# Kernel optimization log

Measured on AMD Instinct MI355X. Metric: run time of the kernel, lower is better.

Reference implementation:

```python
import jax, jax.numpy as jnp
import numpy as np

B, F, H = 512, 64, 256
INPUT_LEN, TARGET_LEN = 128, 128


def _gru_step(h, xt, Wih, Whh, bih, bhh):
    # PyTorch GRU cell: gates ordered [r, z, n]
    gi = xt @ Wih.T + bih            # [B, 3H]
    gh = h @ Whh.T + bhh             # [B, 3H]
    ir, iz, inn = jnp.split(gi, 3, axis=-1)
    hr, hz, hn = jnp.split(gh, 3, axis=-1)
    r = jax.nn.sigmoid(ir + hr)
    z = jax.nn.sigmoid(iz + hz)
    n = jnp.tanh(inn + r * hn)
    return (1.0 - z) * n + z * h


def setup_inputs() -> dict:
    key = jax.random.key(0)
    ks = jax.random.split(key, 12)
    s_in = 1.0 / np.sqrt(H)
    x = jax.random.normal(ks[0], (B, INPUT_LEN + TARGET_LEN, F), dtype=jnp.float32)
    u = lambda k, shp: jax.random.uniform(k, shp, jnp.float32, -s_in, s_in)
    return {
        "x": x,
        "enc_Wih": u(ks[1], (3 * H, F)), "enc_Whh": u(ks[2], (3 * H, H)),
        "enc_bih": u(ks[3], (3 * H,)), "enc_bhh": u(ks[4], (3 * H,)),
        "dec_Wih": u(ks[5], (3 * H, F)), "dec_Whh": u(ks[6], (3 * H, H)),
        "dec_bih": u(ks[7], (3 * H,)), "dec_bhh": u(ks[8], (3 * H,)),
        "reg_W": u(ks[9], (F, H)), "reg_b": u(ks[10], (F,)),
        "input_len": INPUT_LEN, "target_len": TARGET_LEN,
    }


def reference(x, enc_Wih, enc_Whh, enc_bih, enc_bhh,
              dec_Wih, dec_Whh, dec_bih, dec_bhh,
              reg_W, reg_b, input_len, target_len):
    source_seq = x[:, :input_len, :]                       # [B, Tin, F]
    b = source_seq.shape[0]

    # Encoder GRU over source sequence, h0 = 0
    def enc_step(h, xt):
        h = _gru_step(h, xt, enc_Wih, enc_Whh, enc_bih, enc_bhh)
        return h, None
    h0 = jnp.zeros((b, enc_Whh.shape[1]), dtype=x.dtype)
    h_enc, _ = jax.lax.scan(enc_step, h0, source_seq.transpose(1, 0, 2))

    # Decoder: eval mode -> teacher forcing prob 0, always feed back own output
    dec_in0 = source_seq[:, -1, :]                         # [B, F]
    def dec_step(carry, _):
        h, inp = carry
        h = _gru_step(h, inp, dec_Wih, dec_Whh, dec_bih, dec_bhh)
        out = h @ reg_W.T + reg_b                          # [B, F]
        return (h, out), out
    (_, _), outs = jax.lax.scan(dec_step, (h_enc, dec_in0), None, length=target_len)
    return outs.transpose(1, 0, 2)                         # [B, Tout, F]
```

## Files before the change

kernel.cpp:

```cpp
#include <hip/hip_runtime.h>
#include <math.h>

#define Bsz 512
#define Fsz 64
#define Hsz 256
#define TSTEPS 128
#define G3 768

#define BG 16
#define HB 16
#define NBLK 256
#define NTHR 256
#define CNT_STRIDE 512
#define POLLER 192

#define AP 264
#define XAP 72

#define OFF_AH  0
#define OFF_AL  16896
#define OFF_XH  33792
#define OFF_XL  38400
#define OFF_RED 43008
#define OFF_B   75776
#define SMEM_BYTES (OFF_B + 512)

typedef float f32x4 __attribute__((ext_vector_type(4)));
typedef short s16x8 __attribute__((ext_vector_type(8)));
typedef unsigned short u16x4 __attribute__((ext_vector_type(4)));
typedef unsigned int  u32x4 __attribute__((ext_vector_type(4)));

#define MF(a,b,c) __builtin_amdgcn_mfma_f32_16x16x32_bf16(a,b,c,0,0,0)

static __device__ __forceinline__ unsigned short bf16_rne(float f){
    union { float f; unsigned u; } v; v.f = f;
    return (unsigned short)((v.u + 0x7FFFu + ((v.u >> 16) & 1u)) >> 16);
}
static __device__ __forceinline__ float bf16_to_f(unsigned short h){
    union { unsigned u; float f; } v; v.u = ((unsigned)h) << 16; return v.f;
}
static __device__ __forceinline__ void split8(const float* p, s16x8& hi, s16x8& lo){
    #pragma unroll
    for (int t = 0; t < 8; ++t){
        float f = p[t];
        unsigned short h = bf16_rne(f);
        hi[t] = (short)h;
        lo[t] = (short)bf16_rne(f - bf16_to_f(h));
    }
}
static __device__ __forceinline__ float sigmoidf_(float v){ return 1.0f/(1.0f + expf(-v)); }

__device__ __forceinline__ u32x4 load_sys_b128u(const unsigned* p){
    u32x4 r;
    asm volatile("global_load_dwordx4 %0, %1, off sc0 sc1" : "=v"(r) : "v"(p) : "memory");
    return r;
}
__device__ __forceinline__ void store_sys_b32u(unsigned* p, unsigned v){
    asm volatile("global_store_dword %0, %1, off sc0 sc1" :: "v"(p), "v"(v) : "memory");
}
__device__ __forceinline__ int load_sys_i32(const int* p){
    int r;
    asm volatile("global_load_dword %0, %1, off sc0 sc1\n\ts_waitcnt vmcnt(0)"
                 : "=v"(r) : "v"(p) : "memory");
    return r;
}
__device__ __forceinline__ void waitcnt0(){ asm volatile("s_waitcnt vmcnt(0)" ::: "memory"); }
__device__ __forceinline__ void regbar(u32x4& v){ asm volatile("" : "+v"(v)); }

extern "C" __global__ void gru_setup(const float* __restrict__ x,
                                     const float* __restrict__ dWih,
                                     const float* __restrict__ dbih,
                                     const float* __restrict__ regW,
                                     const float* __restrict__ regb,
                                     float* __restrict__ Mw,
                                     float* __restrict__ cfold,
                                     float* __restrict__ gi0)
{
    int idx = blockIdx.x*blockDim.x + threadIdx.x;
    if (idx < G3*Hsz) {
        int g = idx >> 8, j = idx & 255;
        float a = 0.f;
        #pragma unroll 8
        for (int f = 0; f < Fsz; ++f) a += dWih[g*Fsz + f]*regW[f*Hsz + j];
        Mw[idx] = a;
    } else if (idx < G3*Hsz + G3) {
        int g = idx - G3*Hsz;
        float a = dbih[g];
        #pragma unroll 8
        for (int f = 0; f < Fsz; ++f) a += dWih[g*Fsz + f]*regb[f];
        cfold[g] = a;
    } else {
        int e = idx - (G3*Hsz + G3);
        if (e < Bsz*G3) {
            int b = e / G3, g = e - b*G3;
            const float* xp = x + (size_t)b*(256*64) + 127*64;
            float a = dbih[g];
            #pragma unroll 8
            for (int f = 0; f < Fsz; ++f) a += xp[f]*dWih[g*Fsz + f];
            gi0[e] = a;
        }
    }
}

extern "C" __global__ void __launch_bounds__(NTHR, 1)
gru_persistent(const float* __restrict__ x,
               const float* __restrict__ eWih, const float* __restrict__ eWhh,
               const float* __restrict__ ebih, const float* __restrict__ ebhh,
               const float* __restrict__ dWhh, const float* __restrict__ dbhh,
               const float* __restrict__ Mw,   const float* __restrict__ cfold,
               const float* __restrict__ gi0,  const float* __restrict__ regW,
               const float* __restrict__ regb,
               unsigned* __restrict__ hbuf, int* __restrict__ cnt,
               float* __restrict__ out)
{
    extern __shared__ char lds[];
    unsigned short* s_ah = (unsigned short*)(lds + OFF_AH);
    unsigned short* s_al = (unsigned short*)(lds + OFF_AL);
    unsigned short* s_xh = (unsigned short*)(lds + OFF_XH);
    unsigned short* s_xl = (unsigned short*)(lds + OFF_XL);
    float* s_red  = (float*)(lds + OFF_RED);
    float* s_bias = (float*)(lds + OFF_B);
    float* s_dbh  = s_bias + 64;
    float* s_b3   = s_bias + 112;

    const int tid  = threadIdx.x;
    const int wv   = tid >> 6;
    const int lane = tid & 63;
    const int quad = lane >> 4;
    const int lcol = lane & 15;
    const int bg   = blockIdx.x >> 4;
    const int hb   = blockIdx.x & 15;
    const int hcol = hb*16 + lcol;
    int* mycnt = cnt + bg*CNT_STRIDE;
    const f32x4 z4 = {0.f, 0.f, 0.f, 0.f};

    s16x8 wfh[3][2], wfl[3][2];
    s16x8 ufh[3], ufl[3];
    #pragma unroll
    for (int g = 0; g < 3; ++g)
        #pragma unroll
        for (int q = 0; q < 2; ++q)
            split8(eWhh + (size_t)(g*256 + hcol)*256 + wv*64 + q*32 + quad*8,
                   wfh[g][q], wfl[g][q]);
    if (wv < 2){
        #pragma unroll
        for (int g = 0; g < 3; ++g)
            split8(eWih + (size_t)(g*256 + hcol)*64 + wv*32 + quad*8, ufh[g], ufl[g]);
    }
    if (tid < 16){
        int c = hb*16 + tid;
        s_bias[tid]    = ebih[c]       + ebhh[c];
        s_bias[16+tid] = ebih[256+c]   + ebhh[256+c];
        s_bias[32+tid] = ebih[512+c];
        s_bias[48+tid] = ebhh[512+c];
    }
    __syncthreads();

    int parity = 0;

    for (int s = 0; s < TSTEPS; ++s) {
        f32x4 aR[2], aZ[2], aNi[2], aNh[2];
        if (wv == 0){
            float bR = s_bias[lcol], bZ = s_bias[16+lcol];
            float bNi = s_bias[32+lcol], bNh = s_bias[48+lcol];
            #pragma unroll
            for (int m = 0; m < 2; ++m){
                aR[m] = (f32x4){bR,bR,bR,bR}; aZ[m] = (f32x4){bZ,bZ,bZ,bZ};
                aNi[m] = (f32x4){bNi,bNi,bNi,bNi}; aNh[m] = (f32x4){bNh,bNh,bNh,bNh};
            }
        } else {
            #pragma unroll
            for (int m = 0; m < 2; ++m){ aR[m]=z4; aZ[m]=z4; aNi[m]=z4; aNh[m]=z4; }
        }

        #pragma unroll
        for (int jj = 0; jj < 2; ++jj){
            int flat = (wv*2 + jj)*64 + lane;
            int row = flat >> 4, c4 = flat & 15;
            f32x4 xv = *(const f32x4*)(x + (size_t)(bg*32+row)*(256*64) + (size_t)s*64 + c4*4);
            u16x4 xh, xl;
            #pragma unroll
            for (int t = 0; t < 4; ++t){
                unsigned short h = bf16_rne(xv[t]);
                xh[t] = h; xl[t] = bf16_rne(xv[t] - bf16_to_f(h));
            }
            *(u16x4*)(s_xh + row*XAP + c4*4) = xh;
            *(u16x4*)(s_xl + row*XAP + c4*4) = xl;
        }
        __syncthreads();

        if (wv < 2){
            #pragma unroll
            for (int m = 0; m < 2; ++m){
                const int ko = wv*32 + quad*8;
                s16x8 xah = *(const s16x8*)(s_xh + (m*16+lcol)*XAP + ko);
                s16x8 xal = *(const s16x8*)(s_xl + (m*16+lcol)*XAP + ko);
                aR[m]=MF(xah,ufh[0],aR[m]); aR[m]=MF(xah,ufl[0],aR[m]); aR[m]=MF(xal,ufh[0],aR[m]);
                aZ[m]=MF(xah,ufh[1],aZ[m]); aZ[m]=MF(xah,ufl[1],aZ[m]); aZ[m]=MF(xal,ufh[1],aZ[m]);
                aNi[m]=MF(xah,ufh[2],aNi[m]); aNi[m]=MF(xah,ufl[2],aNi[m]); aNi[m]=MF(xal,ufh[2],aNi[m]);
            }
        }

        if (s > 0 && tid == POLLER){
            while (load_sys_i32(mycnt + s) < HB) __builtin_amdgcn_s_sleep(2);
        }
        __syncthreads();

        const unsigned* hin = hbuf + (size_t)parity*Bsz*Hsz;
        {
            u32x4 t[8];
            #pragma unroll
            for (int jj = 0; jj < 8; ++jj){
                int flat = (wv*8 + jj)*64 + lane;
                int row = flat >> 6, c4 = flat & 63;
                t[jj] = load_sys_b128u(hin + (size_t)(bg*32+row)*256 + c4*4);
            }
            waitcnt0();
            #pragma unroll
            for (int jj = 0; jj < 8; ++jj) regbar(t[jj]);
            #pragma unroll
            for (int jj = 0; jj < 8; ++jj){
                int flat = (wv*8 + jj)*64 + lane;
                int row = flat >> 6, c4 = flat & 63;
                u16x4 hh, ll;
                #pragma unroll
                for (int e = 0; e < 4; ++e){
                    unsigned u = t[jj][e];
                    hh[e] = (unsigned short)(u >> 16);
                    ll[e] = (unsigned short)(u & 0xFFFFu);
                }
                *(u16x4*)(s_ah + row*AP + c4*4) = hh;
                *(u16x4*)(s_al + row*AP + c4*4) = ll;
            }
        }
        __syncthreads();

        #pragma unroll
        for (int m = 0; m < 2; ++m){
            #pragma unroll
            for (int q = 0; q < 2; ++q){
                const int ko = wv*64 + q*32 + quad*8;
                s16x8 ah = *(const s16x8*)(s_ah + (m*16+lcol)*AP + ko);
                s16x8 al = *(const s16x8*)(s_al + (m*16+lcol)*AP + ko);
                aR[m]=MF(ah,wfh[0][q],aR[m]); aR[m]=MF(ah,wfl[0][q],aR[m]); aR[m]=MF(al,wfh[0][q],aR[m]);
                aZ[m]=MF(ah,wfh[1][q],aZ[m]); aZ[m]=MF(ah,wfl[1][q],aZ[m]); aZ[m]=MF(al,wfh[1][q],aZ[m]);
                aNh[m]=MF(ah,wfh[2][q],aNh[m]); aNh[m]=MF(ah,wfl[2][q],aNh[m]); aNh[m]=MF(al,wfh[2][q],aNh[m]);
            }
        }

        #pragma unroll
        for (int m = 0; m < 2; ++m){
            f32x4* rp = (f32x4*)s_red + (wv*8 + m*4)*64 + lane;
            rp[0] = aR[m]; rp[64] = aZ[m]; rp[128] = aNi[m]; rp[192] = aNh[m];
        }
        __syncthreads();

        unsigned* hout = hbuf + (size_t)(parity^1)*Bsz*Hsz;
        if (wv < 2){
            const int m = wv;
            f32x4 R = z4, Z = z4, Ni = z4, Nh = z4;
            #pragma unroll
            for (int w = 0; w < 4; ++w){
                const f32x4* rp = (const f32x4*)s_red + (w*8 + m*4)*64 + lane;
                R += rp[0]; Z += rp[64]; Ni += rp[128]; Nh += rp[192];
            }
            #pragma unroll
            for (int j = 0; j < 4; ++j){
                int rl = m*16 + quad*4 + j;
                float r = sigmoidf_(R[j]);
                float z = sigmoidf_(Z[j]);
                float n = tanhf(Ni[j] + r*Nh[j]);
                float hold = bf16_to_f(s_ah[rl*AP + hcol]) + bf16_to_f(s_al[rl*AP + hcol]);
                float hv = (1.0f - z)*n + z*hold;
                unsigned short p1 = bf16_rne(hv);
                unsigned short p0 = bf16_rne(hv - bf16_to_f(p1));
                store_sys_b32u(hout + (size_t)(bg*32+rl)*256 + hcol,
                               (((unsigned)p1) << 16) | (unsigned)p0);
            }
            waitcnt0();
        }
        __syncthreads();
        if (tid == POLLER)
            __hip_atomic_fetch_add(mycnt + s + 1, 1, __ATOMIC_RELAXED,
                                   __HIP_MEMORY_SCOPE_SYSTEM);
        parity ^= 1;
    }

    s16x8 mfh[3][2], mfl[3][2];
    #pragma unroll
    for (int g = 0; g < 3; ++g)
        #pragma unroll
        for (int q = 0; q < 2; ++q){
            split8(dWhh + (size_t)(g*256 + hcol)*256 + wv*64 + q*32 + quad*8,
                   wfh[g][q], wfl[g][q]);
            split8(Mw   + (size_t)(g*256 + hcol)*256 + wv*64 + q*32 + quad*8,
                   mfh[g][q], mfl[g][q]);
        }
    s16x8 rwh[8], rwl[8];
    if (wv >= 2){
        #pragma unroll
        for (int q8 = 0; q8 < 8; ++q8)
            split8(regW + (size_t)(hb*4 + (lcol & 3))*256 + q8*32 + quad*8,
                   rwh[q8], rwl[q8]);
    }
    if (tid < 16){
        int c = hb*16 + tid;
        s_bias[tid]    = cfold[c]     + dbhh[c];
        s_bias[16+tid] = cfold[256+c] + dbhh[256+c];
        s_bias[32+tid] = cfold[512+c];
        s_dbh[tid]     = dbhh[c];
        s_dbh[16+tid]  = dbhh[256+c];
        s_dbh[32+tid]  = dbhh[512+c];
    }
    if (tid < 4) s_b3[tid] = regb[hb*4 + tid];
    __syncthreads();

    for (int i = 0; i < TSTEPS; ++i) {
        const int sflag = TSTEPS + i;

        f32x4 aR[2], aZ[2], aNi[2], aNh[2];
        if (wv == 0){
            if (i == 0){
                #pragma unroll
                for (int m = 0; m < 2; ++m){
                    #pragma unroll
                    for (int j = 0; j < 4; ++j){
                        int grow_ = bg*32 + m*16 + quad*4 + j;
                        const float* gp = gi0 + (size_t)grow_*G3 + hcol;
                        aR[m][j]  = gp[0]   + s_dbh[lcol];
                        aZ[m][j]  = gp[256] + s_dbh[16+lcol];
                        aNi[m][j] = gp[512];
                        aNh[m][j] = s_dbh[32+lcol];
                    }
                }
            } else {
                float bR = s_bias[lcol], bZ = s_bias[16+lcol];
                float bNi = s_bias[32+lcol], bNh = s_dbh[32+lcol];
                #pragma unroll
                for (int m = 0; m < 2; ++m){
                    aR[m] = (f32x4){bR,bR,bR,bR}; aZ[m] = (f32x4){bZ,bZ,bZ,bZ};
                    aNi[m] = (f32x4){bNi,bNi,bNi,bNi}; aNh[m] = (f32x4){bNh,bNh,bNh,bNh};
                }
            }
        } else {
            #pragma unroll
            for (int m = 0; m < 2; ++m){ aR[m]=z4; aZ[m]=z4; aNi[m]=z4; aNh[m]=z4; }
        }

        if (tid == POLLER){
            while (load_sys_i32(mycnt + sflag) < HB) __builtin_amdgcn_s_sleep(2);
        }
        __syncthreads();

        const unsigned* hin = hbuf + (size_t)parity*Bsz*Hsz;
        {
            u32x4 t[8];
            #pragma unroll
            for (int jj = 0; jj < 8; ++jj){
                int flat = (wv*8 + jj)*64 + lane;
                int row = flat >> 6, c4 = flat & 63;
                t[jj] = load_sys_b128u(hin + (size_t)(bg*32+row)*256 + c4*4);
            }
            waitcnt0();
            #pragma unroll
            for (int jj = 0; jj < 8; ++jj) regbar(t[jj]);
            #pragma unroll
            for (int jj = 0; jj < 8; ++jj){
                int flat = (wv*8 + jj)*64 + lane;
                int row = flat >> 6, c4 = flat & 63;
                u16x4 hh, ll;
                #pragma unroll
                for (int e = 0; e < 4; ++e){
                    unsigned u = t[jj][e];
                    hh[e] = (unsigned short)(u >> 16);
                    ll[e] = (unsigned short)(u & 0xFFFFu);
                }
                *(u16x4*)(s_ah + row*AP + c4*4) = hh;
                *(u16x4*)(s_al + row*AP + c4*4) = ll;
            }
        }
        __syncthreads();

        #pragma unroll
        for (int m = 0; m < 2; ++m){
            #pragma unroll
            for (int q = 0; q < 2; ++q){
                const int ko = wv*64 + q*32 + quad*8;
                s16x8 ah = *(const s16x8*)(s_ah + (m*16+lcol)*AP + ko);
                s16x8 al = *(const s16x8*)(s_al + (m*16+lcol)*AP + ko);
                aR[m]=MF(ah,wfh[0][q],aR[m]); aR[m]=MF(ah,wfl[0][q],aR[m]); aR[m]=MF(al,wfh[0][q],aR[m]);
                aZ[m]=MF(ah,wfh[1][q],aZ[m]); aZ[m]=MF(ah,wfl[1][q],aZ[m]); aZ[m]=MF(al,wfh[1][q],aZ[m]);
                aNh[m]=MF(ah,wfh[2][q],aNh[m]); aNh[m]=MF(ah,wfl[2][q],aNh[m]); aNh[m]=MF(al,wfh[2][q],aNh[m]);
                if (i > 0){
                    aR[m]=MF(ah,mfh[0][q],aR[m]); aR[m]=MF(ah,mfl[0][q],aR[m]); aR[m]=MF(al,mfh[0][q],aR[m]);
                    aZ[m]=MF(ah,mfh[1][q],aZ[m]); aZ[m]=MF(ah,mfl[1][q],aZ[m]); aZ[m]=MF(al,mfh[1][q],aZ[m]);
                    aNi[m]=MF(ah,mfh[2][q],aNi[m]); aNi[m]=MF(ah,mfl[2][q],aNi[m]); aNi[m]=MF(al,mfh[2][q],aNi[m]);
                }
            }
        }

        #pragma unroll
        for (int m = 0; m < 2; ++m){
            f32x4* rp = (f32x4*)s_red + (wv*8 + m*4)*64 + lane;
            rp[0] = aR[m]; rp[64] = aZ[m]; rp[128] = aNi[m]; rp[192] = aNh[m];
        }
        __syncthreads();

        unsigned* hout = hbuf + (size_t)(parity^1)*Bsz*Hsz;
        if (wv < 2){
            const int m = wv;
            f32x4 R = z4, Z = z4, Ni = z4, Nh = z4;
            #pragma unroll
            for (int w = 0; w < 4; ++w){
                const f32x4* rp = (const f32x4*)s_red + (w*8 + m*4)*64 + lane;
                R += rp[0]; Z += rp[64]; Ni += rp[128]; Nh += rp[192];
            }
            #pragma unroll
            for (int j = 0; j < 4; ++j){
                int rl = m*16 + quad*4 + j;
                float r = sigmoidf_(R[j]);
                float z = sigmoidf_(Z[j]);
                float n = tanhf(Ni[j] + r*Nh[j]);
                float hold = bf16_to_f(s_ah[rl*AP + hcol]) + bf16_to_f(s_al[rl*AP + hcol]);
                float hv = (1.0f - z)*n + z*hold;
                unsigned short p1 = bf16_rne(hv);
                unsigned short p0 = bf16_rne(hv - bf16_to_f(p1));
                store_sys_b32u(hout + (size_t)(bg*32+rl)*256 + hcol,
                               (((unsigned)p1) << 16) | (unsigned)p0);
            }
            waitcnt0();
        } else if (i >= 1){
            const int m = wv - 2;
            float b3 = s_b3[lcol & 3];
            f32x4 oa = (f32x4){b3, b3, b3, b3};
            #pragma unroll
            for (int q8 = 0; q8 < 8; ++q8){
                const int ko = q8*32 + quad*8;
                s16x8 ah = *(const s16x8*)(s_ah + (m*16+lcol)*AP + ko);
                s16x8 al = *(const s16x8*)(s_al + (m*16+lcol)*AP + ko);
                oa = MF(ah, rwh[q8], oa); oa = MF(ah, rwl[q8], oa); oa = MF(al, rwh[q8], oa);
            }
            if (lcol < 4){
                #pragma unroll
                for (int j = 0; j < 4; ++j)
                    out[(size_t)(bg*32 + m*16 + quad*4 + j)*(TSTEPS*Fsz)
                        + (size_t)(i-1)*Fsz + hb*4 + lcol] = oa[j];
            }
        }
        __syncthreads();
        if (tid == POLLER)
            __hip_atomic_fetch_add(mycnt + sflag + 1, 1, __ATOMIC_RELAXED,
                                   __HIP_MEMORY_SCOPE_SYSTEM);
        parity ^= 1;
    }

    {
        if (tid == POLLER){
            while (load_sys_i32(mycnt + 2*TSTEPS) < HB) __builtin_amdgcn_s_sleep(2);
        }
        __syncthreads();
        const unsigned* hin = hbuf + (size_t)parity*Bsz*Hsz;
        {
            u32x4 t[8];
            #pragma unroll
            for (int jj = 0; jj < 8; ++jj){
                int flat = (wv*8 + jj)*64 + lane;
                int row = flat >> 6, c4 = flat & 63;
                t[jj] = load_sys_b128u(hin + (size_t)(bg*32+row)*256 + c4*4);
            }
            waitcnt0();
            #pragma unroll
            for (int jj = 0; jj < 8; ++jj) regbar(t[jj]);
            #pragma unroll
            for (int jj = 0; jj < 8; ++jj){
                int flat = (wv*8 + jj)*64 + lane;
                int row = flat >> 6, c4 = flat & 63;
                u16x4 hh, ll;
                #pragma unroll
                for (int e = 0; e < 4; ++e){
                    unsigned u = t[jj][e];
                    hh[e] = (unsigned short)(u >> 16);
                    ll[e] = (unsigned short)(u & 0xFFFFu);
                }
                *(u16x4*)(s_ah + row*AP + c4*4) = hh;
                *(u16x4*)(s_al + row*AP + c4*4) = ll;
            }
        }
        __syncthreads();
        if (wv >= 2){
            const int m = wv - 2;
            float b3 = s_b3[lcol & 3];
            f32x4 oa = (f32x4){b3, b3, b3, b3};
            #pragma unroll
            for (int q8 = 0; q8 < 8; ++q8){
                const int ko = q8*32 + quad*8;
                s16x8 ah = *(const s16x8*)(s_ah + (m*16+lcol)*AP + ko);
                s16x8 al = *(const s16x8*)(s_al + (m*16+lcol)*AP + ko);
                oa = MF(ah, rwh[q8], oa); oa = MF(ah, rwl[q8], oa); oa = MF(al, rwh[q8], oa);
            }
            if (lcol < 4){
                #pragma unroll
                for (int j = 0; j < 4; ++j)
                    out[(size_t)(bg*32 + m*16 + quad*4 + j)*(TSTEPS*Fsz)
                        + (size_t)(TSTEPS-1)*Fsz + hb*4 + lcol] = oa[j];
            }
        }
    }
}

extern "C" void kernel_launch(void* const* d_in, const int* in_sizes, int n_in,
                              void* d_out, int out_size, void* d_ws, size_t ws_size,
                              hipStream_t stream)
{
    (void)in_sizes; (void)n_in; (void)out_size; (void)ws_size;
    const float* x    = (const float*)d_in[0];
    const float* eWih = (const float*)d_in[1];
    const float* eWhh = (const float*)d_in[2];
    const float* ebih = (const float*)d_in[3];
    const float* ebhh = (const float*)d_in[4];
    const float* dWih = (const float*)d_in[5];
    const float* dWhh = (const float*)d_in[6];
    const float* dbih = (const float*)d_in[7];
    const float* dbhh = (const float*)d_in[8];
    const float* regW = (const float*)d_in[9];
    const float* regb = (const float*)d_in[10];
    float* out = (float*)d_out;

    unsigned* hbuf = (unsigned*)d_ws;
    float* Mw    = (float*)d_ws + 2*Bsz*Hsz;
    float* gi0   = Mw + G3*Hsz;
    float* cfold = gi0 + Bsz*G3;
    int*   cnt   = (int*)(cfold + 1024);

    hipMemsetAsync(hbuf, 0, (size_t)Bsz*Hsz*sizeof(unsigned), stream);
    hipMemsetAsync(cnt, 0, (size_t)BG*CNT_STRIDE*sizeof(int), stream);

    hipLaunchKernelGGL(gru_setup, dim3(2307), dim3(256), 0, stream,
                       x, dWih, dbih, regW, regb, Mw, cfold, gi0);

    hipFuncSetAttribute((const void*)gru_persistent,
                        hipFuncAttributeMaxDynamicSharedMemorySize, SMEM_BYTES);

    void* args[] = { (void*)&x, (void*)&eWih, (void*)&eWhh, (void*)&ebih, (void*)&ebhh,
                     (void*)&dWhh, (void*)&dbhh, (void*)&Mw, (void*)&cfold, (void*)&gi0,
                     (void*)&regW, (void*)&regb, (void*)&hbuf, (void*)&cnt, (void*)&out };
    hipError_t rc = hipLaunchCooperativeKernel((const void*)gru_persistent,
                                               dim3(NBLK), dim3(NTHR), args,
                                               SMEM_BYTES, stream);
    if (rc != hipSuccess) {
        hipLaunchKernelGGL(gru_persistent, dim3(NBLK), dim3(NTHR), SMEM_BYTES, stream,
                           x, eWih, eWhh, ebih, ebhh, dWhh, dbhh, Mw, cfold, gi0,
                           regW, regb, hbuf, cnt, out);
    }
}
```

Before: 1.185 ms.

## Replace counter barrier with per-wave tags and direct register loads of h

Reworks the persistent GRU step loop. The per-group atomic counter polled by one thread, together with several block-wide __syncthreads per step, is replaced by per-block/half tag words that every wave polls itself. Each wave now loads its own hidden-state rows straight from global memory into registers instead of staging them through LDS. The K dimension is split across wave pairs with a small LDS partial-sum handoff guarded by a workgroup-scope flag, which cuts intra-block barriers and LDS traffic on the serial critical path. The risks are extra redundant global polling and loads, and more register pressure from holding twice as many weight fragments per wave.

```diff
diff --git a/kernel.cpp b/kernel.cpp
--- a/kernel.cpp
+++ b/kernel.cpp
@@ -11,24 +11,10 @@
 #define HB 16
 #define NBLK 256
 #define NTHR 256
-#define CNT_STRIDE 512
-#define POLLER 192
-
-#define AP 264
-#define XAP 72
-
-#define OFF_AH  0
-#define OFF_AL  16896
-#define OFF_XH  33792
-#define OFF_XL  38400
-#define OFF_RED 43008
-#define OFF_B   75776
-#define SMEM_BYTES (OFF_B + 512)
 
 typedef float f32x4 __attribute__((ext_vector_type(4)));
 typedef short s16x8 __attribute__((ext_vector_type(8)));
-typedef unsigned short u16x4 __attribute__((ext_vector_type(4)));
-typedef unsigned int  u32x4 __attribute__((ext_vector_type(4)));
+typedef unsigned int u32x4 __attribute__((ext_vector_type(4)));
 
 #define MF(a,b,c) __builtin_amdgcn_mfma_f32_16x16x32_bf16(a,b,c,0,0,0)
 
@@ -40,19 +26,46 @@
     union { unsigned u; float f; } v; v.u = ((unsigned)h) << 16; return v.f;
 }
 static __device__ __forceinline__ void split8(const float* p, s16x8& hi, s16x8& lo){
+    union { s16x8 v; unsigned short e[8]; } H, L;
     #pragma unroll
     for (int t = 0; t < 8; ++t){
         float f = p[t];
         unsigned short h = bf16_rne(f);
-        hi[t] = (short)h;
-        lo[t] = (short)bf16_rne(f - bf16_to_f(h));
-    }
+        H.e[t] = h; L.e[t] = bf16_rne(f - bf16_to_f(h));
+    }
+    hi = H.v; lo = L.v;
+}
+static __device__ __forceinline__ void split8f(f32x4 a, f32x4 b, s16x8& hi, s16x8& lo){
+    union { s16x8 v; unsigned short e[8]; } H, L;
+    float fv[8] = {a[0],a[1],a[2],a[3],b[0],b[1],b[2],b[3]};
+    #pragma unroll
+    for (int t = 0; t < 8; ++t){
+        unsigned short h = bf16_rne(fv[t]);
+        H.e[t] = h; L.e[t] = bf16_rne(fv[t] - bf16_to_f(h));
+    }
+    hi = H.v; lo = L.v;
+}
+static __device__ __forceinline__ void unpack8(u32x4 a, u32x4 b, s16x8& hi, s16x8& lo){
+    union { s16x8 v; unsigned u[4]; } H, L;
+    unsigned w[8] = {a[0],a[1],a[2],a[3],b[0],b[1],b[2],b[3]};
+    #pragma unroll
+    for (int d = 0; d < 4; ++d){
+        unsigned w0 = w[2*d], w1 = w[2*d+1];
+        H.u[d] = (w0 >> 16) | (w1 & 0xFFFF0000u);
+        L.u[d] = (w0 & 0xFFFFu) | (w1 << 16);
+    }
+    hi = H.v; lo = L.v;
 }
 static __device__ __forceinline__ float sigmoidf_(float v){ return 1.0f/(1.0f + expf(-v)); }
 
 __device__ __forceinline__ u32x4 load_sys_b128u(const unsigned* p){
     u32x4 r;
     asm volatile("global_load_dwordx4 %0, %1, off sc0 sc1" : "=v"(r) : "v"(p) : "memory");
+    return r;
+}
+__device__ __forceinline__ unsigned load_sys_b32u_async(const unsigned* p){
+    unsigned r;
+    asm volatile("global_load_dword %0, %1, off sc0 sc1" : "=v"(r) : "v"(p) : "memory");
     return r;
 }
 __device__ __forceinline__ void store_sys_b32u(unsigned* p, unsigned v){
@@ -65,7 +78,13 @@
     return r;
 }
 __device__ __forceinline__ void waitcnt0(){ asm volatile("s_waitcnt vmcnt(0)" ::: "memory"); }
-__device__ __forceinline__ void regbar(u32x4& v){ asm volatile("" : "+v"(v)); }
+__device__ __forceinline__ void regbar4(u32x4& v){ asm volatile("" : "+v"(v)); }
+__device__ __forceinline__ void regbar1(unsigned& v){ asm volatile("" : "+v"(v)); }
+
+__device__ __forceinline__ void poll_ge(const int* tp, int target){
+    int v;
+    do { v = load_sys_i32(tp); } while (!__all(v >= target));
+}
 
 extern "C" __global__ void gru_setup(const float* __restrict__ x,
                                      const float* __restrict__ dWih,
@@ -110,400 +129,315 @@
                const float* __restrict__ Mw,   const float* __restrict__ cfold,
                const float* __restrict__ gi0,  const float* __restrict__ regW,
                const float* __restrict__ regb,
-               unsigned* __restrict__ hbuf, int* __restrict__ cnt,
+               unsigned* __restrict__ hbuf, int* __restrict__ tags,
                float* __restrict__ out)
 {
-    extern __shared__ char lds[];
-    unsigned short* s_ah = (unsigned short*)(lds + OFF_AH);
-    unsigned short* s_al = (unsigned short*)(lds + OFF_AL);
-    unsigned short* s_xh = (unsigned short*)(lds + OFF_XH);
-    unsigned short* s_xl = (unsigned short*)(lds + OFF_XL);
-    float* s_red  = (float*)(lds + OFF_RED);
-    float* s_bias = (float*)(lds + OFF_B);
-    float* s_dbh  = s_bias + 64;
-    float* s_b3   = s_bias + 112;
+    __shared__ float s_part[4][4][256];
+    __shared__ float s_bias[128];
+    __shared__ unsigned short s_rw[2][8][64][8];
+    __shared__ int s_flag[2];
 
     const int tid  = threadIdx.x;
     const int wv   = tid >> 6;
+    const int m    = wv & 1;
+    const int kh   = wv >> 1;
     const int lane = tid & 63;
     const int quad = lane >> 4;
     const int lcol = lane & 15;
     const int bg   = blockIdx.x >> 4;
     const int hb   = blockIdx.x & 15;
     const int hcol = hb*16 + lcol;
-    int* mycnt = cnt + bg*CNT_STRIDE;
-    const f32x4 z4 = {0.f, 0.f, 0.f, 0.f};
-
-    s16x8 wfh[3][2], wfl[3][2];
+    const int* mytags = tags + bg*32;
+    const f32x4 z4 = {0.f,0.f,0.f,0.f};
+
+    s16x8 wfh[3][4], wfl[3][4];
     s16x8 ufh[3], ufl[3];
     #pragma unroll
-    for (int g = 0; g < 3; ++g)
-        #pragma unroll
-        for (int q = 0; q < 2; ++q)
-            split8(eWhh + (size_t)(g*256 + hcol)*256 + wv*64 + q*32 + quad*8,
-                   wfh[g][q], wfl[g][q]);
-    if (wv < 2){
-        #pragma unroll
-        for (int g = 0; g < 3; ++g)
-            split8(eWih + (size_t)(g*256 + hcol)*64 + wv*32 + quad*8, ufh[g], ufl[g]);
-    }
+    for (int g3 = 0; g3 < 3; ++g3){
+        #pragma unroll
+        for (int q = 0; q < 4; ++q)
+            split8(eWhh + (size_t)(g3*256 + hcol)*256 + kh*128 + q*32 + quad*8,
+                   wfh[g3][q], wfl[g3][q]);
+        split8(eWih + (size_t)(g3*256 + hcol)*64 + kh*32 + quad*8, ufh[g3], ufl[g3]);
+    }
+    if (tid == 0){ s_flag[0] = 0; s_flag[1] = 0; }
     if (tid < 16){
         int c = hb*16 + tid;
-        s_bias[tid]    = ebih[c]       + ebhh[c];
-        s_bias[16+tid] = ebih[256+c]   + ebhh[256+c];
+        s_bias[tid]    = ebih[c]     + ebhh[c];
+        s_bias[16+tid] = ebih[256+c] + ebhh[256+c];
         s_bias[32+tid] = ebih[512+c];
         s_bias[48+tid] = ebhh[512+c];
     }
     __syncthreads();
 
-    int parity = 0;
-
-    for (int s = 0; s < TSTEPS; ++s) {
-        f32x4 aR[2], aZ[2], aNi[2], aNh[2];
-        if (wv == 0){
-            float bR = s_bias[lcol], bZ = s_bias[16+lcol];
-            float bNi = s_bias[32+lcol], bNh = s_bias[48+lcol];
-            #pragma unroll
-            for (int m = 0; m < 2; ++m){
-                aR[m] = (f32x4){bR,bR,bR,bR}; aZ[m] = (f32x4){bZ,bZ,bZ,bZ};
-                aNi[m] = (f32x4){bNi,bNi,bNi,bNi}; aNh[m] = (f32x4){bNh,bNh,bNh,bNh};
-            }
+    for (int g = 0; g < TSTEPS; ++g){
+        const unsigned* hin  = hbuf + (size_t)(g & 1)*Bsz*Hsz;
+        unsigned* hout = hbuf + (size_t)((g + 1) & 1)*Bsz*Hsz;
+
+        f32x4 accR = z4, accZ = z4, accNi = z4, accNh = z4;
+
+        {
+            const float* xp = x + (size_t)(bg*32 + m*16 + lcol)*(256*64)
+                              + (size_t)g*64 + kh*32 + quad*8;
+            f32x4 xa = *(const f32x4*)xp;
+            f32x4 xb = *(const f32x4*)(xp + 4);
+            s16x8 xh, xl; split8f(xa, xb, xh, xl);
+            accR  = MF(xh, ufh[0], accR);  accR  = MF(xh, ufl[0], accR);  accR  = MF(xl, ufh[0], accR);
+            accZ  = MF(xh, ufh[1], accZ);  accZ  = MF(xh, ufl[1], accZ);  accZ  = MF(xl, ufh[1], accZ);
+            accNi = MF(xh, ufh[2], accNi); accNi = MF(xh, ufl[2], accNi); accNi = MF(xl, ufh[2], accNi);
+        }
+
+        if (g > 0) poll_ge(mytags + (lane & 31), g);
+
+        const unsigned* hrow = hin + (size_t)(bg*32 + m*16 + lcol)*256;
+        u32x4 A[8];
+        #pragma unroll
+        for (int q = 0; q < 4; ++q){
+            int ko = kh*128 + q*32 + quad*8;
+            A[2*q]   = load_sys_b128u(hrow + ko);
+            A[2*q+1] = load_sys_b128u(hrow + ko + 4);
+        }
+        unsigned HO[4];
+        if (kh == 0){
+            #pragma unroll
+            for (int j = 0; j < 4; ++j)
+                HO[j] = load_sys_b32u_async(hin + (size_t)(bg*32 + m*16 + quad*4 + j)*256 + hcol);
+        }
+        waitcnt0();
+        #pragma unroll
+        for (int q = 0; q < 8; ++q) regbar4(A[q]);
+        if (kh == 0){ regbar1(HO[0]); regbar1(HO[1]); regbar1(HO[2]); regbar1(HO[3]); }
+
+        s16x8 ah[4], al[4];
+        #pragma unroll
+        for (int q = 0; q < 4; ++q) unpack8(A[2*q], A[2*q+1], ah[q], al[q]);
+
+        #pragma unroll
+        for (int q = 0; q < 4; ++q){
+            s16x8 H = ah[q], L = al[q];
+            accR  = MF(H, wfh[0][q], accR);  accR  = MF(H, wfl[0][q], accR);  accR  = MF(L, wfh[0][q], accR);
+            accZ  = MF(H, wfh[1][q], accZ);  accZ  = MF(H, wfl[1][q], accZ);  accZ  = MF(L, wfh[1][q], accZ);
+            accNh = MF(H, wfh[2][q], accNh); accNh = MF(H, wfl[2][q], accNh); accNh = MF(L, wfh[2][q], accNh);
+        }
+
+        const int par = g & 1;
+        if (kh == 1){
+            float* pb = &s_part[m*2 + par][0][0] + lane*4;
+            *(f32x4*)(pb)       = accR;
+            *(f32x4*)(pb + 256) = accZ;
+            *(f32x4*)(pb + 512) = accNi;
+            *(f32x4*)(pb + 768) = accNh;
+            if (lane == 0)
+                __hip_atomic_store(&s_flag[m], g + 1, __ATOMIC_RELEASE, __HIP_MEMORY_SCOPE_WORKGROUP);
         } else {
-            #pragma unroll
-            for (int m = 0; m < 2; ++m){ aR[m]=z4; aZ[m]=z4; aNi[m]=z4; aNh[m]=z4; }
-        }
-
-        #pragma unroll
-        for (int jj = 0; jj < 2; ++jj){
-            int flat = (wv*2 + jj)*64 + lane;
-            int row = flat >> 4, c4 = flat & 15;
-            f32x4 xv = *(const f32x4*)(x + (size_t)(bg*32+row)*(256*64) + (size_t)s*64 + c4*4);
-            u16x4 xh, xl;
-            #pragma unroll
-            for (int t = 0; t < 4; ++t){
-                unsigned short h = bf16_rne(xv[t]);
-                xh[t] = h; xl[t] = bf16_rne(xv[t] - bf16_to_f(h));
-            }
-            *(u16x4*)(s_xh + row*XAP + c4*4) = xh;
-            *(u16x4*)(s_xl + row*XAP + c4*4) = xl;
-        }
-        __syncthreads();
-
-        if (wv < 2){
-            #pragma unroll
-            for (int m = 0; m < 2; ++m){
-                const int ko = wv*32 + quad*8;
-                s16x8 xah = *(const s16x8*)(s_xh + (m*16+lcol)*XAP + ko);
-                s16x8 xal = *(const s16x8*)(s_xl + (m*16+lcol)*XAP + ko);
-                aR[m]=MF(xah,ufh[0],aR[m]); aR[m]=MF(xah,ufl[0],aR[m]); aR[m]=MF(xal,ufh[0],aR[m]);
-                aZ[m]=MF(xah,ufh[1],aZ[m]); aZ[m]=MF(xah,ufl[1],aZ[m]); aZ[m]=MF(xal,ufh[1],aZ[m]);
-                aNi[m]=MF(xah,ufh[2],aNi[m]); aNi[m]=MF(xah,ufl[2],aNi[m]); aNi[m]=MF(xal,ufh[2],aNi[m]);
-            }
-        }
-
-        if (s > 0 && tid == POLLER){
-            while (load_sys_i32(mycnt + s) < HB) __builtin_amdgcn_s_sleep(2);
-        }
-        __syncthreads();
-
-        const unsigned* hin = hbuf + (size_t)parity*Bsz*Hsz;
-        {
-            u32x4 t[8];
-            #pragma unroll
-            for (int jj = 0; jj < 8; ++jj){
-                int flat = (wv*8 + jj)*64 + lane;
-                int row = flat >> 6, c4 = flat & 63;
-                t[jj] = load_sys_b128u(hin + (size_t)(bg*32+row)*256 + c4*4);
-            }
-            waitcnt0();
-            #pragma unroll
-            for (int jj = 0; jj < 8; ++jj) regbar(t[jj]);
-            #pragma unroll
-            for (int jj = 0; jj < 8; ++jj){
-                int flat = (wv*8 + jj)*64 + lane;
-                int row = flat >> 6, c4 = flat & 63;
-                u16x4 hh, ll;
-                #pragma unroll
-                for (int e = 0; e < 4; ++e){
-                    unsigned u = t[jj][e];
-                    hh[e] = (unsigned short)(u >> 16);
-                    ll[e] = (unsigned short)(u & 0xFFFFu);
-                }
-                *(u16x4*)(s_ah + row*AP + c4*4) = hh;
-                *(u16x4*)(s_al + row*AP + c4*4) = ll;
-            }
-        }
-        __syncthreads();
-
-        #pragma unroll
-        for (int m = 0; m < 2; ++m){
-            #pragma unroll
-            for (int q = 0; q < 2; ++q){
-                const int ko = wv*64 + q*32 + quad*8;
-                s16x8 ah = *(const s16x8*)(s_ah + (m*16+lcol)*AP + ko);
-                s16x8 al = *(const s16x8*)(s_al + (m*16+lcol)*AP + ko);
-                aR[m]=MF(ah,wfh[0][q],aR[m]); aR[m]=MF(ah,wfl[0][q],aR[m]); aR[m]=MF(al,wfh[0][q],aR[m]);
-                aZ[m]=MF(ah,wfh[1][q],aZ[m]); aZ[m]=MF(ah,wfl[1][q],aZ[m]); aZ[m]=MF(al,wfh[1][q],aZ[m]);
-                aNh[m]=MF(ah,wfh[2][q],aNh[m]); aNh[m]=MF(ah,wfl[2][q],aNh[m]); aNh[m]=MF(al,wfh[2][q],aNh[m]);
-            }
-        }
-
-        #pragma unroll
-        for (int m = 0; m < 2; ++m){
-            f32x4* rp = (f32x4*)s_red + (wv*8 + m*4)*64 + lane;
-            rp[0] = aR[m]; rp[64] = aZ[m]; rp[128] = aNi[m]; rp[192] = aNh[m];
-        }
-        __syncthreads();
-
-        unsigned* hout = hbuf + (size_t)(parity^1)*Bsz*Hsz;
-        if (wv < 2){
-            const int m = wv;
-            f32x4 R = z4, Z = z4, Ni = z4, Nh = z4;
-            #pragma unroll
-            for (int w = 0; w < 4; ++w){
-                const f32x4* rp = (const f32x4*)s_red + (w*8 + m*4)*64 + lane;
-                R += rp[0]; Z += rp[64]; Ni += rp[128]; Nh += rp[192];
-            }
+            while (__hip_atomic_load(&s_flag[m], __ATOMIC_ACQUIRE, __HIP_MEMORY_SCOPE_WORKGROUP) < g + 1) {}
+            const float* pb = &s_part[m*2 + par][0][0] + lane*4;
+            accR  += *(const f32x4*)(pb);
+            accZ  += *(const f32x4*)(pb + 256);
+            accNi += *(const f32x4*)(pb + 512);
+            accNh += *(const f32x4*)(pb + 768);
             #pragma unroll
             for (int j = 0; j < 4; ++j){
-                int rl = m*16 + quad*4 + j;
-                float r = sigmoidf_(R[j]);
-                float z = sigmoidf_(Z[j]);
-                float n = tanhf(Ni[j] + r*Nh[j]);
-                float hold = bf16_to_f(s_ah[rl*AP + hcol]) + bf16_to_f(s_al[rl*AP + hcol]);
-                float hv = (1.0f - z)*n + z*hold;
+                float R = sigmoidf_(accR[j] + s_bias[lcol]);
+                float Z = sigmoidf_(accZ[j] + s_bias[16 + lcol]);
+                float N = tanhf(accNi[j] + s_bias[32 + lcol] + R*(accNh[j] + s_bias[48 + lcol]));
+                float hold = bf16_to_f((unsigned short)(HO[j] >> 16))
+                           + bf16_to_f((unsigned short)(HO[j] & 0xFFFFu));
+                float hv = (1.0f - Z)*N + Z*hold;
                 unsigned short p1 = bf16_rne(hv);
                 unsigned short p0 = bf16_rne(hv - bf16_to_f(p1));
-                store_sys_b32u(hout + (size_t)(bg*32+rl)*256 + hcol,
+                store_sys_b32u(hout + (size_t)(bg*32 + m*16 + quad*4 + j)*256 + hcol,
                                (((unsigned)p1) << 16) | (unsigned)p0);
             }
             waitcnt0();
-        }
-        __syncthreads();
-        if (tid == POLLER)
-            __hip_atomic_fetch_add(mycnt + s + 1, 1, __ATOMIC_RELAXED,
-                                   __HIP_MEMORY_SCOPE_SYSTEM);
-        parity ^= 1;
-    }
-
-    s16x8 mfh[3][2], mfl[3][2];
+            if (lane == 0)
+                store_sys_b32u((unsigned*)(tags + bg*32 + hb*2 + m), (unsigned)(g + 1));
+        }
+    }
+
+    __syncthreads();
+    s16x8 mfh[3][4], mfl[3][4];
     #pragma unroll
-    for (int g = 0; g < 3; ++g)
-        #pragma unroll
-        for (int q = 0; q < 2; ++q){
-            split8(dWhh + (size_t)(g*256 + hcol)*256 + wv*64 + q*32 + quad*8,
-                   wfh[g][q], wfl[g][q]);
-            split8(Mw   + (size_t)(g*256 + hcol)*256 + wv*64 + q*32 + quad*8,
-                   mfh[g][q], mfl[g][q]);
-        }
-    s16x8 rwh[8], rwl[8];
-    if (wv >= 2){
-        #pragma unroll
-        for (int q8 = 0; q8 < 8; ++q8)
-            split8(regW + (size_t)(hb*4 + (lcol & 3))*256 + q8*32 + quad*8,
-                   rwh[q8], rwl[q8]);
+    for (int g3 = 0; g3 < 3; ++g3)
+        #pragma unroll
+        for (int q = 0; q < 4; ++q){
+            split8(dWhh + (size_t)(g3*256 + hcol)*256 + kh*128 + q*32 + quad*8,
+                   wfh[g3][q], wfl[g3][q]);
+            split8(Mw   + (size_t)(g3*256 + hcol)*256 + kh*128 + q*32 + quad*8,
+                   mfh[g3][q], mfl[g3][q]);
+        }
+    if (wv == 2){
+        #pragma unroll
+        for (int q8 = 0; q8 < 8; ++q8){
+            s16x8 rh, rl;
+            split8(regW + (size_t)(hb*4 + (lcol & 3))*256 + q8*32 + quad*8, rh, rl);
+            *(s16x8*)&s_rw[0][q8][lane][0] = rh;
+            *(s16x8*)&s_rw[1][q8][lane][0] = rl;
+        }
     }
     if (tid < 16){
         int c = hb*16 + tid;
-        s_bias[tid]    = cfold[c]     + dbhh[c];
-        s_bias[16+tid] = cfold[256+c] + dbhh[256+c];
-        s_bias[32+tid] = cfold[512+c];
-        s_dbh[tid]     = dbhh[c];
-        s_dbh[16+tid]  = dbhh[256+c];
-        s_dbh[32+tid]  = dbhh[512+c];
-    }
-    if (tid < 4) s_b3[tid] = regb[hb*4 + tid];
+        s_bias[tid]      = cfold[c]       + dbhh[c];
+        s_bias[16+tid]   = cfold[256+c]   + dbhh[256+c];
+        s_bias[32+tid]   = cfold[512+c];
+        s_bias[48+tid]   = dbhh[512+c];
+        s_bias[64+tid]   = dbhh[c];
+        s_bias[80+tid]   = dbhh[256+c];
+    }
+    if (tid < 4) s_bias[96 + tid] = regb[hb*4 + tid];
     __syncthreads();
 
-    for (int i = 0; i < TSTEPS; ++i) {
-        const int sflag = TSTEPS + i;
-
-        f32x4 aR[2], aZ[2], aNi[2], aNh[2];
-        if (wv == 0){
-            if (i == 0){
+    for (int i = 0; i < TSTEPS; ++i){
+        const int g = TSTEPS + i;
+        const unsigned* hin  = hbuf + (size_t)(g & 1)*Bsz*Hsz;
+        unsigned* hout = hbuf + (size_t)((g + 1) & 1)*Bsz*Hsz;
+
+        f32x4 accR = z4, accZ = z4, accNi = z4, accNh = z4;
+
+        poll_ge(mytags + (lane & 31), g);
+
+        const unsigned* hrow = hin + (size_t)(bg*32 + m*16 + lcol)*256;
+        u32x4 A[8], B2[8];
+        #pragma unroll
+        for (int q = 0; q < 4; ++q){
+            int ko = kh*128 + q*32 + quad*8;
+            A[2*q]   = load_sys_b128u(hrow + ko);
+            A[2*q+1] = load_sys_b128u(hrow + ko + 4);
+        }
+        unsigned HO[4];
+        if (kh == 0){
+            #pragma unroll
+            for (int j = 0; j < 4; ++j)
+                HO[j] = load_sys_b32u_async(hin + (size_t)(bg*32 + m*16 + quad*4 + j)*256 + hcol);
+        } else if (i >= 1){
+            #pragma unroll
+            for (int q = 0; q < 4; ++q){
+                int ko = q*32 + quad*8;
+                B2[2*q]   = load_sys_b128u(hrow + ko);
+                B2[2*q+1] = load_sys_b128u(hrow + ko + 4);
+            }
+        }
+        waitcnt0();
+        #pragma unroll
+        for (int q = 0; q < 8; ++q) regbar4(A[q]);
+        if (kh == 0){ regbar1(HO[0]); regbar1(HO[1]); regbar1(HO[2]); regbar1(HO[3]); }
+        else if (i >= 1){
+            #pragma unroll
+            for (int q = 0; q < 8; ++q) regbar4(B2[q]);
+        }
+
+        s16x8 ah[4], al[4];
+        #pragma unroll
+        for (int q = 0; q < 4; ++q) unpack8(A[2*q], A[2*q+1], ah[q], al[q]);
+
+        #pragma unroll
+        for (int q = 0; q < 4; ++q){
+            s16x8 H = ah[q], L = al[q];
+            accR  = MF(H, wfh[0][q], accR);  accR  = MF(H, wfl[0][q], accR);  accR  = MF(L, wfh[0][q], accR);
+            accZ  = MF(H, wfh[1][q], accZ);  accZ  = MF(H, wfl[1][q], accZ);  accZ  = MF(L, wfh[1][q], accZ);
+            accNh = MF(H, wfh[2][q], accNh); accNh = MF(H, wfl[2][q], accNh); accNh = MF(L, wfh[2][q], accNh);
+        }
+        if (i > 0){
+            #pragma unroll
+            for (int q = 0; q < 4; ++q){
+                s16x8 H = ah[q], L = al[q];
+                accR  = MF(H, mfh[0][q], accR);  accR  = MF(H, mfl[0][q], accR);  accR  = MF(L, mfh[0][q], accR);
+                accZ  = MF(H, mfh[1][q], accZ);  accZ  = MF(H, mfl[1][q], accZ);  accZ  = MF(L, mfh[1][q], accZ);
+                accNi = MF(H, mfh[2][q], accNi); accNi = MF(H, mfl[2][q], accNi); accNi = MF(L, mfh[2][q], accNi);
+            }
+        }
+
+        const int par = g & 1;
+        if (kh == 1){
+            float* pb = &s_part[m*2 + par][0][0] + lane*4;
+            *(f32x4*)(pb)       = accR;
+            *(f32x4*)(pb + 256) = accZ;
+            *(f32x4*)(pb + 512) = accNi;
+            *(f32x4*)(pb + 768) = accNh;
+            if (lane == 0)
+                __hip_atomic_store(&s_flag[m], g + 1, __ATOMIC_RELEASE, __HIP_MEMORY_SCOPE_WORKGROUP);
+            if (i >= 1){
+                s16x8 bh[4], bl[4];
                 #pragma unroll
-                for (int m = 0; m < 2; ++m){
+                for (int q = 0; q < 4; ++q) unpack8(B2[2*q], B2[2*q+1], bh[q], bl[q]);
+                float b3 = s_bias[96 + (lcol & 3)];
+                f32x4 oa = (f32x4){b3, b3, b3, b3};
+                #pragma unroll
+                for (int q8 = 0; q8 < 8; ++q8){
+                    s16x8 H = (q8 < 4) ? bh[q8] : ah[q8-4];
+                    s16x8 L = (q8 < 4) ? bl[q8] : al[q8-4];
+                    s16x8 rh = *(const s16x8*)&s_rw[0][q8][lane][0];
+                    s16x8 rl = *(const s16x8*)&s_rw[1][q8][lane][0];
+                    oa = MF(H, rh, oa); oa = MF(H, rl, oa); oa = MF(L, rh, oa);
+                }
+                if (lcol < 4){
                     #pragma unroll
-                    for (int j = 0; j < 4; ++j){
-                        int grow_ = bg*32 + m*16 + quad*4 + j;
-                        const float* gp = gi0 + (size_t)grow_*G3 + hcol;
-                        aR[m][j]  = gp[0]   + s_dbh[lcol];
-                        aZ[m][j]  = gp[256] + s_dbh[16+lcol];
-                        aNi[m][j] = gp[512];
-                        aNh[m][j] = s_dbh[32+lcol];
-                    }
-                }
-            } else {
-                float bR = s_bias[lcol], bZ = s_bias[16+lcol];
-                float bNi = s_bias[32+lcol], bNh = s_dbh[32+lcol];
-                #pragma unroll
-                for (int m = 0; m < 2; ++m){
-                    aR[m] = (f32x4){bR,bR,bR,bR}; aZ[m] = (f32x4){bZ,bZ,bZ,bZ};
-                    aNi[m] = (f32x4){bNi,bNi,bNi,bNi}; aNh[m] = (f32x4){bNh,bNh,bNh,bNh};
+                    for (int j = 0; j < 4; ++j)
+                        out[(size_t)(bg*32 + m*16 + quad*4 + j)*(TSTEPS*Fsz)
+                            + (size_t)(i-1)*Fsz + hb*4 + lcol] = oa[j];
                 }
             }
         } else {
-            #pragma unroll
-            for (int m = 0; m < 2; ++m){ aR[m]=z4; aZ[m]=z4; aNi[m]=z4; aNh[m]=z4; }
-        }
-
-        if (tid == POLLER){
-            while (load_sys_i32(mycnt + sflag) < HB) __builtin_amdgcn_s_sleep(2);
-        }
-        __syncthreads();
-
-        const unsigned* hin = hbuf + (size_t)parity*Bsz*Hsz;
-        {
-            u32x4 t[8];
-            #pragma unroll
-            for (int jj = 0; jj < 8; ++jj){
-                int flat = (wv*8 + jj)*64 + lane;
-                int row = flat >> 6, c4 = flat & 63;
-                t[jj] = load_sys_b128u(hin + (size_t)(bg*32+row)*256 + c4*4);
-            }
-            waitcnt0();
-            #pragma unroll
-            for (int jj = 0; jj < 8; ++jj) regbar(t[jj]);
-            #pragma unroll
-            for (int jj = 0; jj < 8; ++jj){
-                int flat = (wv*8 + jj)*64 + lane;
-                int row = flat >> 6, c4 = flat & 63;
-                u16x4 hh, ll;
-                #pragma unroll
-                for (int e = 0; e < 4; ++e){
-                    unsigned u = t[jj][e];
-                    hh[e] = (unsigned short)(u >> 16);
-                    ll[e] = (unsigned short)(u & 0xFFFFu);
+            while (__hip_atomic_load(&s_flag[m], __ATOMIC_ACQUIRE, __HIP_MEMORY_SCOPE_WORKGROUP) < g + 1) {}
+            const float* pb = &s_part[m*2 + par][0][0] + lane*4;
+            accR  += *(const f32x4*)(pb);
+            accZ  += *(const f32x4*)(pb + 256);
+            accNi += *(const f32x4*)(pb + 512);
+            accNh += *(const f32x4*)(pb + 768);
+            #pragma unroll
+            for (int j = 0; j < 4; ++j){
+                float R, Z, N;
+                if (i == 0){
+                    const float* gp = gi0 + (size_t)(bg*32 + m*16 + quad*4 + j)*G3 + hcol;
+                    R = sigmoidf_(accR[j] + gp[0]   + s_bias[64 + lcol]);
+                    Z = sigmoidf_(accZ[j] + gp[256] + s_bias[80 + lcol]);
+                    N = tanhf(accNi[j] + gp[512] + R*(accNh[j] + s_bias[48 + lcol]));
+                } else {
+                    R = sigmoidf_(accR[j] + s_bias[lcol]);
+                    Z = sigmoidf_(accZ[j] + s_bias[16 + lcol]);
+                    N = tanhf(accNi[j] + s_bias[32 + lcol] + R*(accNh[j] + s_bias[48 + lcol]));
                 }
-                *(u16x4*)(s_ah + row*AP + c4*4) = hh;
-                *(u16x4*)(s_al + row*AP + c4*4) = ll;
-            }
-        }
-        __syncthreads();
-
-        #pragma unroll
-        for (int m = 0; m < 2; ++m){
-            #pragma unroll
-            for (int q = 0; q < 2; ++q){
-                const int ko = wv*64 + q*32 + quad*8;
-                s16x8 ah = *(const s16x8*)(s_ah + (m*16+lcol)*AP + ko);
-                s16x8 al = *(const s16x8*)(s_al + (m*16+lcol)*AP + ko);
-                aR[m]=MF(ah,wfh[0][q],aR[m]); aR[m]=MF(ah,wfl[0][q],aR[m]); aR[m]=MF(al,wfh[0][q],aR[m]);
-                aZ[m]=MF(ah,wfh[1][q],aZ[m]); aZ[m]=MF(ah,wfl[1][q],aZ[m]); aZ[m]=MF(al,wfh[1][q],aZ[m]);
-                aNh[m]=MF(ah,wfh[2][q],aNh[m]); aNh[m]=MF(ah,wfl[2][q],aNh[m]); aNh[m]=MF(al,wfh[2][q],aNh[m]);
-                if (i > 0){
-                    aR[m]=MF(ah,mfh[0][q],aR[m]); aR[m]=MF(ah,mfl[0][q],aR[m]); aR[m]=MF(al,mfh[0][q],aR[m]);
-                    aZ[m]=MF(ah,mfh[1][q],aZ[m]); aZ[m]=MF(ah,mfl[1][q],aZ[m]); aZ[m]=MF(al,mfh[1][q],aZ[m]);
-                    aNi[m]=MF(ah,mfh[2][q],aNi[m]); aNi[m]=MF(ah,mfl[2][q],aNi[m]); aNi[m]=MF(al,mfh[2][q],aNi[m]);
-                }
-            }
-        }
-
-        #pragma unroll
-        for (int m = 0; m < 2; ++m){
-            f32x4* rp = (f32x4*)s_red + (wv*8 + m*4)*64 + lane;
-            rp[0] = aR[m]; rp[64] = aZ[m]; rp[128] = aNi[m]; rp[192] = aNh[m];
-        }
-        __syncthreads();
-
-        unsigned* hout = hbuf + (size_t)(parity^1)*Bsz*Hsz;
-        if (wv < 2){
-            const int m = wv;
-            f32x4 R = z4, Z = z4, Ni = z4, Nh = z4;
-            #pragma unroll
-            for (int w = 0; w < 4; ++w){
-                const f32x4* rp = (const f32x4*)s_red + (w*8 + m*4)*64 + lane;
-                R += rp[0]; Z += rp[64]; Ni += rp[128]; Nh += rp[192];
-            }
-            #pragma unroll
-            for (int j = 0; j < 4; ++j){
-                int rl = m*16 + quad*4 + j;
-                float r = sigmoidf_(R[j]);
-                float z = sigmoidf_(Z[j]);
-                float n = tanhf(Ni[j] + r*Nh[j]);
-                float hold = bf16_to_f(s_ah[rl*AP + hcol]) + bf16_to_f(s_al[rl*AP + hcol]);
-                float hv = (1.0f - z)*n + z*hold;
+                float hold = bf16_to_f((unsigned short)(HO[j] >> 16))
+                           + bf16_to_f((unsigned short)(HO[j] & 0xFFFFu));
+                float hv = (1.0f - Z)*N + Z*hold;
                 unsigned short p1 = bf16_rne(hv);
                 unsigned short p0 = bf16_rne(hv - bf16_to_f(p1));
-                store_sys_b32u(hout + (size_t)(bg*32+rl)*256 + hcol,
+                store_sys_b32u(hout + (size_t)(bg*32 + m*16 + quad*4 + j)*256 + hcol,
                                (((unsigned)p1) << 16) | (unsigned)p0);
             }
             waitcnt0();
-        } else if (i >= 1){
-            const int m = wv - 2;
-            float b3 = s_b3[lcol & 3];
-            f32x4 oa = (f32x4){b3, b3, b3, b3};
-            #pragma unroll
-            for (int q8 = 0; q8 < 8; ++q8){
-                const int ko = q8*32 + quad*8;
-                s16x8 ah = *(const s16x8*)(s_ah + (m*16+lcol)*AP + ko);
-                s16x8 al = *(const s16x8*)(s_al + (m*16+lcol)*AP + ko);
-                oa = MF(ah, rwh[q8], oa); oa = MF(ah, rwl[q8], oa); oa = MF(al, rwh[q8], oa);
-            }
-            if (lcol < 4){
-                #pragma unroll
-                for (int j = 0; j < 4; ++j)
-                    out[(size_t)(bg*32 + m*16 + quad*4 + j)*(TSTEPS*Fsz)
-                        + (size_t)(i-1)*Fsz + hb*4 + lcol] = oa[j];
-            }
-        }
-        __syncthreads();
-        if (tid == POLLER)
-            __hip_atomic_fetch_add(mycnt + sflag + 1, 1, __ATOMIC_RELAXED,
-                                   __HIP_MEMORY_SCOPE_SYSTEM);
-        parity ^= 1;
-    }
-
-    {
-        if (tid == POLLER){
-            while (load_sys_i32(mycnt + 2*TSTEPS) < HB) __builtin_amdgcn_s_sleep(2);
-        }
-        __syncthreads();
-        const unsigned* hin = hbuf + (size_t)parity*Bsz*Hsz;
-        {
-            u32x4 t[8];
-            #pragma unroll
-            for (int jj = 0; jj < 8; ++jj){
-                int flat = (wv*8 + jj)*64 + lane;
-                int row = flat >> 6, c4 = flat & 63;
-                t[jj] = load_sys_b128u(hin + (size_t)(bg*32+row)*256 + c4*4);
-            }
-            waitcnt0();
-            #pragma unroll
-            for (int jj = 0; jj < 8; ++jj) regbar(t[jj]);
-            #pragma unroll
-            for (int jj = 0; jj < 8; ++jj){
-                int flat = (wv*8 + jj)*64 + lane;
-                int row = flat >> 6, c4 = flat & 63;
-                u16x4 hh, ll;
-                #pragma unroll
-                for (int e = 0; e < 4; ++e){
-                    unsigned u = t[jj][e];
-                    hh[e] = (unsigned short)(u >> 16);
-                    ll[e] = (unsigned short)(u & 0xFFFFu);
-                }
-                *(u16x4*)(s_ah + row*AP + c4*4) = hh;
-                *(u16x4*)(s_al + row*AP + c4*4) = ll;
-            }
-        }
-        __syncthreads();
-        if (wv >= 2){
-            const int m = wv - 2;
-            float b3 = s_b3[lcol & 3];
-            f32x4 oa = (f32x4){b3, b3, b3, b3};
-            #pragma unroll
-            for (int q8 = 0; q8 < 8; ++q8){
-                const int ko = q8*32 + quad*8;
-                s16x8 ah = *(const s16x8*)(s_ah + (m*16+lcol)*AP + ko);
-                s16x8 al = *(const s16x8*)(s_al + (m*16+lcol)*AP + ko);
-                oa = MF(ah, rwh[q8], oa); oa = MF(ah, rwl[q8], oa); oa = MF(al, rwh[q8], oa);
-            }
-            if (lcol < 4){
-                #pragma unroll
-                for (int j = 0; j < 4; ++j)
-                    out[(size_t)(bg*32 + m*16 + quad*4 + j)*(TSTEPS*Fsz)
-                        + (size_t)(TSTEPS-1)*Fsz + hb*4 + lcol] = oa[j];
-            }
+            if (lane == 0)
+                store_sys_b32u((unsigned*)(tags + bg*32 + hb*2 + m), (unsigned)(g + 1));
+        }
+    }
+
+    if (kh == 1){
+        poll_ge(mytags + (lane & 31), 2*TSTEPS);
+        const unsigned* hrow = hbuf + (size_t)(bg*32 + m*16 + lcol)*256;
+        u32x4 C[16];
+        #pragma unroll
+        for (int q8 = 0; q8 < 8; ++q8){
+            int ko = q8*32 + quad*8;
+            C[2*q8]   = load_sys_b128u(hrow + ko);
+            C[2*q8+1] = load_sys_b128u(hrow + ko + 4);
+        }
+        waitcnt0();
+        #pragma unroll
+        for (int q = 0; q < 16; ++q) regbar4(C[q]);
+        float b3 = s_bias[96 + (lcol & 3)];
+        f32x4 oa = (f32x4){b3, b3, b3, b3};
+        #pragma unroll
+        for (int q8 = 0; q8 < 8; ++q8){
+            s16x8 H, L; unpack8(C[2*q8], C[2*q8+1], H, L);
+            s16x8 rh = *(const s16x8*)&s_rw[0][q8][lane][0];
+            s16x8 rl = *(const s16x8*)&s_rw[1][q8][lane][0];
+            oa = MF(H, rh, oa); oa = MF(H, rl, oa); oa = MF(L, rh, oa);
+        }
+        if (lcol < 4){
+            #pragma unroll
+            for (int j = 0; j < 4; ++j)
+                out[(size_t)(bg*32 + m*16 + quad*4 + j)*(TSTEPS*Fsz)
+                    + (size_t)(TSTEPS-1)*Fsz + hb*4 + lcol] = oa[j];
         }
     }
 }
@@ -530,26 +464,22 @@
     float* Mw    = (float*)d_ws + 2*Bsz*Hsz;
     float* gi0   = Mw + G3*Hsz;
     float* cfold = gi0 + Bsz*G3;
-    int*   cnt   = (int*)(cfold + 1024);
+    int*   tags  = (int*)(cfold + 1024);
 
     hipMemsetAsync(hbuf, 0, (size_t)Bsz*Hsz*sizeof(unsigned), stream);
-    hipMemsetAsync(cnt, 0, (size_t)BG*CNT_STRIDE*sizeof(int), stream);
+    hipMemsetAsync(tags, 0, (size_t)BG*32*sizeof(int), stream);
 
     hipLaunchKernelGGL(gru_setup, dim3(2307), dim3(256), 0, stream,
                        x, dWih, dbih, regW, regb, Mw, cfold, gi0);
 
-    hipFuncSetAttribute((const void*)gru_persistent,
-                        hipFuncAttributeMaxDynamicSharedMemorySize, SMEM_BYTES);
-
     void* args[] = { (void*)&x, (void*)&eWih, (void*)&eWhh, (void*)&ebih, (void*)&ebhh,
                      (void*)&dWhh, (void*)&dbhh, (void*)&Mw, (void*)&cfold, (void*)&gi0,
-                     (void*)&regW, (void*)&regb, (void*)&hbuf, (void*)&cnt, (void*)&out };
+                     (void*)&regW, (void*)&regb, (void*)&hbuf, (void*)&tags, (void*)&out };
     hipError_t rc = hipLaunchCooperativeKernel((const void*)gru_persistent,
-                                               dim3(NBLK), dim3(NTHR), args,
-                                               SMEM_BYTES, stream);
+                                               dim3(NBLK), dim3(NTHR), args, 0, stream);
     if (rc != hipSuccess) {
-        hipLaunchKernelGGL(gru_persistent, dim3(NBLK), dim3(NTHR), SMEM_BYTES, stream,
+        hipLaunchKernelGGL(gru_persistent, dim3(NBLK), dim3(NTHR), 0, stream,
                            x, eWih, eWhh, ebih, ebhh, dWhh, dbhh, Mw, cfold, gi0,
-                           regW, regb, hbuf, cnt, out);
-    }
-}
+                           regW, regb, hbuf, tags, out);
+    }
+}
```

Result: slower. 1.651 ms (+39.3%).
